# Kernel optimization log

Measured on AMD Instinct MI355X. Metric: run time of the kernel, lower is better.

The kernel has to match this reference:

```python
import jax, jax.numpy as jnp
import numpy as np

B, L, D_MODEL, H, D_K, D_V = 64, 52, 4096, 32, 128, 128
NEW_C = D_MODEL // H  # per-head input channel after the (faithful) raw reshape


def setup_inputs() -> dict:
    key = jax.random.key(0)
    ks = jax.random.split(key, 12)
    s = 0.02
    return {
        "Q": jax.random.normal(ks[0], (B, L, D_MODEL), jnp.float32),
        "K": jax.random.normal(ks[1], (B, L, D_MODEL), jnp.float32),
        "V": jax.random.normal(ks[2], (B, L, D_MODEL), jnp.float32),
        "Wq": jax.random.normal(ks[3], (H, NEW_C, D_K), jnp.float32) * s,
        "bq": jnp.zeros((H, D_K), jnp.float32),
        "Wk": jax.random.normal(ks[4], (H, NEW_C, D_K), jnp.float32) * s,
        "bk": jnp.zeros((H, D_K), jnp.float32),
        "Wv": jax.random.normal(ks[5], (H, NEW_C, D_V), jnp.float32) * s,
        "bv": jnp.zeros((H, D_V), jnp.float32),
        "Wo": jax.random.normal(ks[6], (H * D_V, D_MODEL), jnp.float32) * s,
        "bo": jnp.zeros((D_MODEL,), jnp.float32),
    }


def reference(Q, K, V, Wq, bq, Wk, bk, Wv, bv, Wo, bo):
    # Faithful to source: raw reshape (B, L, D) -> (B, H, L, D/H), NOT a channel split.
    def split(x):
        return x.reshape(B, H, L, NEW_C)

    q = jnp.einsum('bhlc,hck->bhlk', split(Q), Wq) + bq[None, :, None, :]  # (B,H,L,D_K)
    k = jnp.einsum('bhlc,hck->bhlk', split(K), Wk) + bk[None, :, None, :]
    v = jnp.einsum('bhlc,hcv->bhlv', split(V), Wv) + bv[None, :, None, :]

    scores = jnp.einsum('bhqk,bhmk->bhqm', q, k) / jnp.sqrt(jnp.asarray(D_K, q.dtype))
    # causal mask: keep j <= i, else -inf (matches the numpy masking loop)
    causal = jnp.tril(jnp.ones((L, L), bool))
    scores = jnp.where(causal[None, None], scores, -jnp.inf)
    attn = jax.nn.softmax(scores, axis=-1)
    o = jnp.einsum('bhqm,bhmv->bhqv', attn, v)  # (B,H,L,D_V)
    o = o.transpose(0, 2, 1, 3).reshape(B, L, H * D_V)  # concat heads on last axis
    # Dropout(0.1) is identity at inference.
    return o @ Wo + bo
```

## Files before the change

kernel.cpp:

```cpp
#include <hip/hip_runtime.h>
#include <hip/hip_bf16.h>

#define B_SZ   64
#define L_SZ   52
#define DMODEL 4096
#define H_SZ   32
#define C_SZ   128
#define DK     128

#define GM 3328
#define GN 4096
#define GK 4096

typedef __bf16 bf16x8 __attribute__((ext_vector_type(8)));
typedef float  f32x4  __attribute__((ext_vector_type(4)));

__device__ __forceinline__ void gload_lds16(const void* g, void* l) {
  __builtin_amdgcn_global_load_lds(
      (__attribute__((address_space(1))) void*)(void*)g,
      (__attribute__((address_space(3))) void*)l, 16, 0, 0);
}

__device__ __forceinline__ unsigned short bfbits(float x) {
  union { __hip_bfloat16 h; unsigned short u; } c;
  c.h = __float2bfloat16(x);
  return c.u;
}

__global__ __launch_bounds__(256) void w3_transpose_kernel(
    const float* __restrict__ Wq, const float* __restrict__ Wk,
    const float* __restrict__ Wv, __hip_bfloat16* __restrict__ WqT,
    __hip_bfloat16* __restrict__ WkT, __hip_bfloat16* __restrict__ WvT) {
  __shared__ float tile[64][65];
  const int bz = blockIdx.z;
  const float* in = (bz < 32 ? Wq : (bz < 64 ? Wk : Wv)) + (size_t)(bz & 31) * 16384;
  __hip_bfloat16* out = (bz < 32 ? WqT : (bz < 64 ? WkT : WvT)) + (size_t)(bz & 31) * 16384;
  const int nt = blockIdx.x, mt = blockIdx.y;
  const int t = threadIdx.x;
  const int r  = t >> 4;
  const int c4 = (t & 15) << 2;
#pragma unroll
  for (int p = 0; p < 4; ++p) {
    const int rr = r + p * 16;
    const float4 v = *(const float4*)(in + (size_t)(mt * 64 + rr) * 128 + nt * 64 + c4);
    tile[rr][c4 + 0] = v.x; tile[rr][c4 + 1] = v.y;
    tile[rr][c4 + 2] = v.z; tile[rr][c4 + 3] = v.w;
  }
  __syncthreads();
#pragma unroll
  for (int p = 0; p < 4; ++p) {
    const int rr = r + p * 16;
    union { __hip_bfloat16 h[4]; ushort4 u; } o4;
#pragma unroll
    for (int e = 0; e < 4; ++e) o4.h[e] = __float2bfloat16(tile[c4 + e][rr]);
    *(ushort4*)(out + (size_t)(nt * 64 + rr) * 128 + mt * 64 + c4) = o4.u;
  }
}

__device__ __forceinline__ void proj_lds(
    const __hip_bfloat16* __restrict__ xs, const __hip_bfloat16* __restrict__ WT,
    const float* __restrict__ bias, __hip_bfloat16* __restrict__ out,
    int n0, int r16, int kq) {
  f32x4 acc[4][2] = {};
  bf16x8 bfrag[2][4];
#pragma unroll
  for (int nt = 0; nt < 2; ++nt)
#pragma unroll
    for (int kk = 0; kk < 4; ++kk)
      bfrag[nt][kk] = *(const bf16x8*)(WT + (n0 + nt * 16 + r16) * 128 + kk * 32 + kq * 8);
#pragma unroll
  for (int kk = 0; kk < 4; ++kk) {
    bf16x8 a[4];
#pragma unroll
    for (int mt = 0; mt < 4; ++mt) {
      const int row = mt * 16 + r16;
      const int rowc = row < 52 ? row : 51;
      a[mt] = *(const bf16x8*)(xs + rowc * 136 + kk * 32 + kq * 8);
    }
#pragma unroll
    for (int mt = 0; mt < 4; ++mt)
#pragma unroll
      for (int nt = 0; nt < 2; ++nt)
        acc[mt][nt] = __builtin_amdgcn_mfma_f32_16x16x32_bf16(a[mt], bfrag[nt][kk], acc[mt][nt], 0, 0, 0);
  }
#pragma unroll
  for (int nt = 0; nt < 2; ++nt) {
    const int col = n0 + nt * 16 + r16;
    const float bv = bias[col];
#pragma unroll
    for (int mt = 0; mt < 4; ++mt) {
      const int m0 = mt * 16 + kq * 4;
      if (m0 < 52) {
#pragma unroll
        for (int i = 0; i < 4; ++i)
          if (m0 + i < 52)
            out[(m0 + i) * 136 + col] = __float2bfloat16(acc[mt][nt][i] + bv);
      }
    }
  }
}

__device__ __forceinline__ uint2 shfl64(uint2 v, int lane) {
  uint2 r;
  r.x = (unsigned)__shfl((int)v.x, lane);
  r.y = (unsigned)__shfl((int)v.y, lane);
  return r;
}

__global__ __launch_bounds__(256, 3) void attn_fused_kernel(
    const float* __restrict__ Qin, const float* __restrict__ Kin,
    const float* __restrict__ Vin,
    const __hip_bfloat16* __restrict__ WqT, const float* __restrict__ bq,
    const __hip_bfloat16* __restrict__ WkT, const float* __restrict__ bk,
    const __hip_bfloat16* __restrict__ WvT, const float* __restrict__ bv,
    __hip_bfloat16* __restrict__ Oc,
    const float* __restrict__ Wo, __hip_bfloat16* __restrict__ WoT) {
  __shared__ __align__(16) char lds[42432];
  const int gid = blockIdx.x;
  const int t = threadIdx.x;

  if (gid >= 2048) {
    float* tile = (float*)lds;
    const int bid2 = gid - 2048;
    const int nt = bid2 & 63, mt = bid2 >> 6;
    const int r  = t >> 4;
    const int c4 = (t & 15) << 2;
#pragma unroll
    for (int p = 0; p < 4; ++p) {
      const int rr = r + p * 16;
      const float4 v = *(const float4*)(Wo + (size_t)(mt * 64 + rr) * 4096 + nt * 64 + c4);
      tile[rr * 65 + c4 + 0] = v.x; tile[rr * 65 + c4 + 1] = v.y;
      tile[rr * 65 + c4 + 2] = v.z; tile[rr * 65 + c4 + 3] = v.w;
    }
    __syncthreads();
#pragma unroll
    for (int p = 0; p < 4; ++p) {
      const int rr = r + p * 16;
      union { __hip_bfloat16 h[4]; ushort4 u; } o4;
#pragma unroll
      for (int e = 0; e < 4; ++e) o4.h[e] = __float2bfloat16(tile[(c4 + e) * 65 + rr]);
      *(ushort4*)(WoT + (size_t)(nt * 64 + rr) * 4096 + mt * 64 + c4) = o4.u;
    }
    return;
  }

  __hip_bfloat16* r0 = (__hip_bfloat16*)(lds);
  __hip_bfloat16* r1 = (__hip_bfloat16*)(lds + 14144);
  __hip_bfloat16* r2 = (__hip_bfloat16*)(lds + 28288);
  float*          s_sh = (float*)(lds + 14144);
  __hip_bfloat16* p_sh = r0;

  const int h = gid & 31, bb = gid >> 5;
  const int lane = t & 63;
  const int w = t >> 6;
  const int r16 = lane & 15, kq = lane >> 4;
  const size_t xoff = (size_t)bb * (L_SZ * DMODEL) + (size_t)h * (L_SZ * C_SZ);
  const int n0 = w * 32;

  {
    const float* xp[3] = {Qin + xoff, Kin + xoff, Vin + xoff};
    __hip_bfloat16* xd[3] = {r0, r1, r2};
#pragma unroll
    for (int tz = 0; tz < 3; ++tz) {
      const float* X = xp[tz];
      __hip_bfloat16* xs = xd[tz];
      for (int idx = t; idx < 52 * 32; idx += 256) {
        const int row = idx >> 5, c4 = (idx & 31) << 2;
        const float4 v = *(const float4*)(X + row * 128 + c4);
        union { __hip_bfloat16 h[4]; ushort4 u; } o4;
        o4.h[0] = __float2bfloat16(v.x); o4.h[1] = __float2bfloat16(v.y);
        o4.h[2] = __float2bfloat16(v.z); o4.h[3] = __float2bfloat16(v.w);
        *(ushort4*)(xs + row * 136 + c4) = o4.u;
      }
    }
  }
  __syncthreads();

  uint2 vb[4][2];
  {
    f32x4 acc[4][2] = {};
    bf16x8 bfrag[2][4];
    const __hip_bfloat16* WT = WvT + (size_t)h * 16384;
#pragma unroll
    for (int nt = 0; nt < 2; ++nt)
#pragma unroll
      for (int kk = 0; kk < 4; ++kk)
        bfrag[nt][kk] = *(const bf16x8*)(WT + (n0 + nt * 16 + r16) * 128 + kk * 32 + kq * 8);
#pragma unroll
    for (int kk = 0; kk < 4; ++kk) {
      bf16x8 a[4];
#pragma unroll
      for (int mt = 0; mt < 4; ++mt) {
        const int row = mt * 16 + r16;
        const int rowc = row < 52 ? row : 51;
        a[mt] = *(const bf16x8*)(r2 + rowc * 136 + kk * 32 + kq * 8);
      }
#pragma unroll
      for (int mt = 0; mt < 4; ++mt)
#pragma unroll
        for (int nt = 0; nt < 2; ++nt)
          acc[mt][nt] = __builtin_amdgcn_mfma_f32_16x16x32_bf16(a[mt], bfrag[nt][kk], acc[mt][nt], 0, 0, 0);
    }
#pragma unroll
    for (int nt = 0; nt < 2; ++nt) {
      const float bvv = bv[h * 128 + n0 + nt * 16 + r16];
#pragma unroll
      for (int mt = 0; mt < 4; ++mt) {
        vb[mt][nt].x = (unsigned)bfbits(acc[mt][nt][0] + bvv) |
                       ((unsigned)bfbits(acc[mt][nt][1] + bvv) << 16);
        vb[mt][nt].y = (unsigned)bfbits(acc[mt][nt][2] + bvv) |
                       ((unsigned)bfbits(acc[mt][nt][3] + bvv) << 16);
      }
    }
  }
  __syncthreads();

  proj_lds(r0, WqT + (size_t)h * 16384, bq + h * 128, r2, n0, r16, kq);
  __syncthreads();

  proj_lds(r1, WkT + (size_t)h * 16384, bk + h * 128, r0, n0, r16, kq);
  __syncthreads();

  {
    const int nq = w * 16;
    f32x4 sacc[4] = {};
#pragma unroll
    for (int kk = 0; kk < 4; ++kk) {
      const int krow = nq + r16;
      const int krc = krow < 52 ? krow : 51;
      const bf16x8 bf_ = *(const bf16x8*)(r0 + krc * 136 + kk * 32 + kq * 8);
#pragma unroll
      for (int mt = 0; mt < 4; ++mt) {
        const int qrow = mt * 16 + r16;
        const int qrc = qrow < 52 ? qrow : 51;
        const bf16x8 a = *(const bf16x8*)(r2 + qrc * 136 + kk * 32 + kq * 8);
        sacc[mt] = __builtin_amdgcn_mfma_f32_16x16x32_bf16(a, bf_, sacc[mt], 0, 0, 0);
      }
    }
    const float scale = 0.08838834764831845f;
#pragma unroll
    for (int mt = 0; mt < 4; ++mt)
#pragma unroll
      for (int i = 0; i < 4; ++i) {
        const int row = mt * 16 + kq * 4 + i;
        if (row < 52) s_sh[row * 68 + nq + r16] = sacc[mt][i] * scale;
      }
  }
  __syncthreads();

  {
    const int r = t >> 2, qd = t & 3;
    if (r < 52) {
      float v[16];
      float mx = -3e38f;
#pragma unroll
      for (int j4 = 0; j4 < 4; ++j4) {
        const f32x4 s4 = *(const f32x4*)(s_sh + r * 68 + qd * 16 + j4 * 4);
#pragma unroll
        for (int e = 0; e < 4; ++e) {
          const int col = qd * 16 + j4 * 4 + e;
          const float val = (col <= r) ? s4[e] : -3e38f;
          v[j4 * 4 + e] = val;
          mx = fmaxf(mx, val);
        }
      }
      mx = fmaxf(mx, __shfl_xor(mx, 1));
      mx = fmaxf(mx, __shfl_xor(mx, 2));
      float ex[16];
      float sum = 0.f;
#pragma unroll
      for (int j = 0; j < 16; ++j) {
        const int col = qd * 16 + j;
        const float e = (col <= r) ? __expf(v[j] - mx) : 0.f;
        ex[j] = e; sum += e;
      }
      sum += __shfl_xor(sum, 1);
      sum += __shfl_xor(sum, 2);
      const float inv = 1.0f / sum;
      union { __hip_bfloat16 h[8]; uint4 q; } p0, p1;
#pragma unroll
      for (int j = 0; j < 8; ++j) {
        p0.h[j] = __float2bfloat16(ex[j] * inv);
        p1.h[j] = __float2bfloat16(ex[8 + j] * inv);
      }
      *(uint4*)(p_sh + r * 72 + qd * 16)     = p0.q;
      *(uint4*)(p_sh + r * 72 + qd * 16 + 8) = p1.q;
    }
  }
  __syncthreads();

  {
    const int half = (kq >> 1) & 1;
    const int src0 = ((kq & 1) << 5) + r16;
    const int src1 = src0 + 16;
    f32x4 oacc[4][2] = {};
#pragma unroll
    for (int kk = 0; kk < 2; ++kk) {
      bf16x8 bfr[2];
#pragma unroll
      for (int nt = 0; nt < 2; ++nt) {
        const uint2 a0 = shfl64(vb[2 * kk + 0][nt], src0);
        const uint2 a1 = shfl64(vb[2 * kk + 1][nt], src0);
        const uint2 b0 = shfl64(vb[2 * kk + 0][nt], src1);
        const uint2 b1 = shfl64(vb[2 * kk + 1][nt], src1);
        union { unsigned u[4]; bf16x8 v; } asm_;
        asm_.u[0] = half ? a1.x : a0.x;
        asm_.u[1] = half ? a1.y : a0.y;
        asm_.u[2] = half ? b1.x : b0.x;
        asm_.u[3] = half ? b1.y : b0.y;
        bfr[nt] = asm_.v;
      }
#pragma unroll
      for (int mt = 0; mt < 4; ++mt) {
        const int prow = mt * 16 + r16;
        const int prc = prow < 52 ? prow : 51;
        const bf16x8 a = *(const bf16x8*)(p_sh + prc * 72 + kk * 32 + kq * 8);
#pragma unroll
        for (int nt = 0; nt < 2; ++nt)
          oacc[mt][nt] = __builtin_amdgcn_mfma_f32_16x16x32_bf16(a, bfr[nt], oacc[mt][nt], 0, 0, 0);
      }
    }
    const size_t obase = (size_t)bb * 52 * 4096 + (size_t)h * 128;
#pragma unroll
    for (int nt = 0; nt < 2; ++nt) {
      const int col = n0 + nt * 16 + r16;
#pragma unroll
      for (int mt = 0; mt < 4; ++mt) {
        const int row0 = mt * 16 + kq * 4;
#pragma unroll
        for (int i = 0; i < 4; ++i) {
          const int row = row0 + i;
          if (row < 52)
            Oc[obase + (size_t)row * 4096 + col] = __float2bfloat16(oacc[mt][nt][i]);
        }
      }
    }
  }
}

#define STAGE(GBASE, REGOFF, KT, KS, WB) do {                                  \
    const __hip_bfloat16* s_ = (GBASE) + (size_t)(KT) * 64 + (KS) * 32;        \
    char* d_ = (WB) + (REGOFF) + ((KS) ? 16384 : 0) + t * 16;                  \
    gload_lds16(s_, d_);                                                       \
    gload_lds16(s_ + (size_t)128 * GK, d_ + 8192);                             \
  } while (0)

#define MFMA16(MQ, BF)                                                         \
  __builtin_amdgcn_sched_barrier(0);                                           \
  __builtin_amdgcn_s_setprio(1);                                               \
  _Pragma("unroll")                                                            \
  for (int mf = 0; mf < 4; ++mf)                                               \
    _Pragma("unroll")                                                          \
    for (int nf = 0; nf < 4; ++nf)                                             \
      acc[(MQ) * 4 + mf][nf] = __builtin_amdgcn_mfma_f32_16x16x32_bf16(        \
          af[mf], BF[nf], acc[(MQ) * 4 + mf][nf], 0, 0, 0);                    \
  __builtin_amdgcn_s_setprio(0)

#define READ_AF(RB, KS, MQ)                                                    \
  _Pragma("unroll")                                                            \
  for (int mf = 0; mf < 4; ++mf)                                               \
    af[mf] = *(const bf16x8*)((RB) + (KS) * 16384 + (MQ) * 4096 + aB0 + mf * 1024)

#define READ_BF(RB, BF, KS)                                                    \
  _Pragma("unroll")                                                            \
  for (int nf = 0; nf < 4; ++nf)                                               \
    BF[nf] = *(const bf16x8*)((RB) + 32768 + (KS) * 16384 + bB0 + nf * 1024)

#define KTILE_BODY(KT, RB, OB) do {                                            \
    const int s1 = (KT) + 1 < 64 ? (KT) + 1 : 63;                              \
    const int s2 = (KT) + 2 < 64 ? (KT) + 2 : 63;                              \
    {                                                                          \
      bf16x8 af[4];                                                            \
      READ_AF(RB, 0, 0);                                                       \
      READ_BF(RB, bf0, 0);                                                     \
      STAGE(gA0, 0, s1, 1, OB);                                                \
      __builtin_amdgcn_s_barrier();                                            \
      asm volatile("s_waitcnt lgkmcnt(0)" ::: "memory");                       \
      MFMA16(0, bf0);                                                          \
      __builtin_amdgcn_s_barrier();                                            \
    }                                                                          \
    {                                                                          \
      bf16x8 af[4];                                                            \
      READ_AF(RB, 0, 1);                                                       \
      STAGE(gB0, 32768, s2, 0, RB);                                            \
      __builtin_amdgcn_s_barrier();                                            \
      asm volatile("s_waitcnt lgkmcnt(0)" ::: "memory");                       \
      MFMA16(1, bf0);                                                          \
      __builtin_amdgcn_s_barrier();                                            \
    }                                                                          \
    {                                                                          \
      bf16x8 af[4];                                                            \
      READ_AF(RB, 1, 0);                                                       \
      READ_BF(RB, bf1, 1);                                                     \
      STAGE(gA0, 0, s2, 0, RB);                                                \
      __builtin_amdgcn_s_barrier();                                            \
      asm volatile("s_waitcnt lgkmcnt(0)" ::: "memory");                       \
      MFMA16(0, bf1);                                                          \
      __builtin_amdgcn_s_barrier();                                            \
    }                                                                          \
    {                                                                          \
      bf16x8 af[4];                                                            \
      READ_AF(RB, 1, 1);                                                       \
      STAGE(gB0, 32768, s2, 1, RB);                                            \
      __builtin_amdgcn_s_barrier();                                            \
      asm volatile("s_waitcnt lgkmcnt(0)" ::: "memory");                       \
      MFMA16(1, bf1);                                                          \
      asm volatile("s_waitcnt vmcnt(6)" ::: "memory");                         \
      __builtin_amdgcn_s_barrier();                                            \
    }                                                                          \
  } while (0)

__global__ __launch_bounds__(512, 2) void out_gemm_kernel(
    const __hip_bfloat16* __restrict__ A, const __hip_bfloat16* __restrict__ Bt,
    const float* __restrict__ bias, float* __restrict__ C) {
  __shared__ __align__(16) char lds[131072];

  int bid = blockIdx.x;
  bid = (bid & 7) * 26 + (bid >> 3);
  const int tm = bid >> 4;
  const int tn = bid & 15;

  const int t = threadIdx.x;
  const int w = t >> 6, lane = t & 63;
  const int wm = w >> 2, wn = w & 3;
  const int r16 = lane & 15, kq = lane >> 4;

  const int srow = t >> 2;
  const int sgslot = (t & 3) ^ ((srow >> 1) & 3);
  const __hip_bfloat16* gA0 = A  + (size_t)(tm * 256 + srow) * GK + sgslot * 8;
  const __hip_bfloat16* gB0 = Bt + (size_t)(tn * 256 + srow) * GK + sgslot * 8;

  const int slotr = kq ^ ((r16 >> 1) & 3);
  const int aB0 = (wm * 128 + r16) * 64 + slotr * 16;
  const int bB0 = (wn * 64 + r16) * 64 + slotr * 16;

  f32x4 acc[8][4] = {};
  bf16x8 bf0[4], bf1[4];

  char* const buf0 = lds;
  char* const buf1 = lds + 65536;

  STAGE(gA0, 0,     0, 0, buf0);
  STAGE(gA0, 0,     0, 1, buf0);
  STAGE(gB0, 32768, 0, 0, buf0);
  STAGE(gB0, 32768, 0, 1, buf0);
  STAGE(gB0, 32768, 1, 0, buf1);
  STAGE(gA0, 0,     1, 0, buf1);
  STAGE(gB0, 32768, 1, 1, buf1);
  asm volatile("s_waitcnt vmcnt(6)" ::: "memory");
  __builtin_amdgcn_s_barrier();

#pragma unroll 1
  for (int kt2 = 0; kt2 < 32; ++kt2) {
    const int kt = kt2 * 2;
    KTILE_BODY(kt,     buf0, buf1);
    KTILE_BODY(kt + 1, buf1, buf0);
  }
  asm volatile("s_waitcnt vmcnt(0) lgkmcnt(0)" ::: "memory");

  const int row0 = tm * 256 + wm * 128 + kq * 4;
  const int col0 = tn * 256 + wn * 64 + r16;
#pragma unroll
  for (int nf = 0; nf < 4; ++nf) {
    const int col = col0 + nf * 16;
    const float bv = bias[col];
#pragma unroll
    for (int mf = 0; mf < 8; ++mf) {
      const int row = row0 + mf * 16;
#pragma unroll
      for (int i = 0; i < 4; ++i)
        C[(size_t)(row + i) * GN + col] = acc[mf][nf][i] + bv;
    }
  }
}

extern "C" void kernel_launch(void* const* d_in, const int* in_sizes, int n_in,
                              void* d_out, int out_size, void* d_ws, size_t ws_size,
                              hipStream_t stream) {
  const float* Q  = (const float*)d_in[0];
  const float* K  = (const float*)d_in[1];
  const float* V  = (const float*)d_in[2];
  const float* Wq = (const float*)d_in[3];
  const float* bq = (const float*)d_in[4];
  const float* Wk = (const float*)d_in[5];
  const float* bk = (const float*)d_in[6];
  const float* Wv = (const float*)d_in[7];
  const float* bv = (const float*)d_in[8];
  const float* Wo = (const float*)d_in[9];
  const float* bo = (const float*)d_in[10];
  float* out = (float*)d_out;

  char* wsb = (char*)d_ws;
  __hip_bfloat16* WoT = (__hip_bfloat16*)wsb;
  __hip_bfloat16* Oc  = (__hip_bfloat16*)(wsb + (size_t)GN * GK * 2);
  __hip_bfloat16* WqT = (__hip_bfloat16*)(wsb + (size_t)GN * GK * 2 + (size_t)GM * GN * 2);
  __hip_bfloat16* WkT = WqT + (size_t)H_SZ * C_SZ * DK;
  __hip_bfloat16* WvT = WkT + (size_t)H_SZ * C_SZ * DK;

  w3_transpose_kernel<<<dim3(2, 2, 96), 256, 0, stream>>>(Wq, Wk, Wv, WqT, WkT, WvT);
  attn_fused_kernel<<<dim3(2048 + 4096), 256, 0, stream>>>(
      Q, K, V, WqT, bq, WkT, bk, WvT, bv, Oc, Wo, WoT);
  out_gemm_kernel<<<dim3(13 * 16), 512, 0, stream>>>(Oc, WoT, bo, out);
}
```

Baseline: 192.4 us.

## Swizzle attention LDS tiles and transpose MFMA operands for vectorized stores

Replaces padded LDS row strides with XOR-swizzled layouts for the Q/K/V, score and probability tiles. Those tiles shrink, so LDS per block drops and launch bounds rise from 3 to 4 blocks per CU. The Q/K projection and the P·V product swap MFMA operand order so each lane holds 4 consecutive columns. That allows packed 8-byte stores to LDS and to global Oc instead of scalar 2-byte stores. The aim is fewer bank conflicts, fewer store instructions and higher occupancy, at the risk of register pressure under the tighter launch bound.

```diff
diff --git a/kernel.cpp b/kernel.cpp
--- a/kernel.cpp
+++ b/kernel.cpp
@@ -25,6 +25,13 @@
   union { __hip_bfloat16 h; unsigned short u; } c;
   c.h = __float2bfloat16(x);
   return c.u;
+}
+
+__device__ __forceinline__ int hwoff(int row, int g) {
+  return row * 128 + ((g ^ (row & 7)) << 3);
+}
+__device__ __forceinline__ int wdoff(int row, int g) {
+  return row * 64 + ((g ^ (row & 7)) << 2);
 }
 
 __global__ __launch_bounds__(256) void w3_transpose_kernel(
@@ -57,44 +64,47 @@
   }
 }
 
-__device__ __forceinline__ void proj_lds(
+__device__ __forceinline__ void proj_swz(
     const __hip_bfloat16* __restrict__ xs, const __hip_bfloat16* __restrict__ WT,
     const float* __restrict__ bias, __hip_bfloat16* __restrict__ out,
     int n0, int r16, int kq) {
-  f32x4 acc[4][2] = {};
-  bf16x8 bfrag[2][4];
-#pragma unroll
-  for (int nt = 0; nt < 2; ++nt)
+  f32x4 acc[2][4] = {};
+  bf16x8 wf[2][4];
+#pragma unroll
+  for (int ct = 0; ct < 2; ++ct)
 #pragma unroll
     for (int kk = 0; kk < 4; ++kk)
-      bfrag[nt][kk] = *(const bf16x8*)(WT + (n0 + nt * 16 + r16) * 128 + kk * 32 + kq * 8);
+      wf[ct][kk] = *(const bf16x8*)(WT + (n0 + ct * 16 + r16) * 128 + kk * 32 + kq * 8);
 #pragma unroll
   for (int kk = 0; kk < 4; ++kk) {
-    bf16x8 a[4];
-#pragma unroll
-    for (int mt = 0; mt < 4; ++mt) {
-      const int row = mt * 16 + r16;
+    bf16x8 xf[4];
+#pragma unroll
+    for (int rt = 0; rt < 4; ++rt) {
+      const int row = rt * 16 + r16;
       const int rowc = row < 52 ? row : 51;
-      a[mt] = *(const bf16x8*)(xs + rowc * 136 + kk * 32 + kq * 8);
-    }
-#pragma unroll
-    for (int mt = 0; mt < 4; ++mt)
-#pragma unroll
-      for (int nt = 0; nt < 2; ++nt)
-        acc[mt][nt] = __builtin_amdgcn_mfma_f32_16x16x32_bf16(a[mt], bfrag[nt][kk], acc[mt][nt], 0, 0, 0);
-  }
-#pragma unroll
-  for (int nt = 0; nt < 2; ++nt) {
-    const int col = n0 + nt * 16 + r16;
-    const float bv = bias[col];
-#pragma unroll
-    for (int mt = 0; mt < 4; ++mt) {
-      const int m0 = mt * 16 + kq * 4;
-      if (m0 < 52) {
-#pragma unroll
-        for (int i = 0; i < 4; ++i)
-          if (m0 + i < 52)
-            out[(m0 + i) * 136 + col] = __float2bfloat16(acc[mt][nt][i] + bv);
+      xf[rt] = *(const bf16x8*)(xs + hwoff(rowc, 4 * kk + kq));
+    }
+#pragma unroll
+    for (int ct = 0; ct < 2; ++ct)
+#pragma unroll
+      for (int rt = 0; rt < 4; ++rt)
+        acc[ct][rt] = __builtin_amdgcn_mfma_f32_16x16x32_bf16(wf[ct][kk], xf[rt], acc[ct][rt], 0, 0, 0);
+  }
+#pragma unroll
+  for (int ct = 0; ct < 2; ++ct) {
+    const int col0 = n0 + ct * 16 + kq * 4;
+    const float4 b4 = *(const float4*)(bias + col0);
+    const int g = (n0 >> 3) + ct * 2 + (kq >> 1);
+#pragma unroll
+    for (int rt = 0; rt < 4; ++rt) {
+      const int row = rt * 16 + r16;
+      if (row < 52) {
+        ushort4 o;
+        o.x = bfbits(acc[ct][rt][0] + b4.x);
+        o.y = bfbits(acc[ct][rt][1] + b4.y);
+        o.z = bfbits(acc[ct][rt][2] + b4.z);
+        o.w = bfbits(acc[ct][rt][3] + b4.w);
+        *(ushort4*)(out + hwoff(row, g) + (kq & 1) * 4) = o;
       }
     }
   }
@@ -107,7 +117,7 @@
   return r;
 }
 
-__global__ __launch_bounds__(256, 3) void attn_fused_kernel(
+__global__ __launch_bounds__(256, 4) void attn_fused_kernel(
     const float* __restrict__ Qin, const float* __restrict__ Kin,
     const float* __restrict__ Vin,
     const __hip_bfloat16* __restrict__ WqT, const float* __restrict__ bq,
@@ -115,7 +125,7 @@
     const __hip_bfloat16* __restrict__ WvT, const float* __restrict__ bv,
     __hip_bfloat16* __restrict__ Oc,
     const float* __restrict__ Wo, __hip_bfloat16* __restrict__ WoT) {
-  __shared__ __align__(16) char lds[42432];
+  __shared__ __align__(16) char lds[39936];
   const int gid = blockIdx.x;
   const int t = threadIdx.x;
 
@@ -145,9 +155,9 @@
   }
 
   __hip_bfloat16* r0 = (__hip_bfloat16*)(lds);
-  __hip_bfloat16* r1 = (__hip_bfloat16*)(lds + 14144);
-  __hip_bfloat16* r2 = (__hip_bfloat16*)(lds + 28288);
-  float*          s_sh = (float*)(lds + 14144);
+  __hip_bfloat16* r1 = (__hip_bfloat16*)(lds + 13312);
+  __hip_bfloat16* r2 = (__hip_bfloat16*)(lds + 26624);
+  float*          s_sh = (float*)(lds + 13312);
   __hip_bfloat16* p_sh = r0;
 
   const int h = gid & 31, bb = gid >> 5;
@@ -170,7 +180,7 @@
         union { __hip_bfloat16 h[4]; ushort4 u; } o4;
         o4.h[0] = __float2bfloat16(v.x); o4.h[1] = __float2bfloat16(v.y);
         o4.h[2] = __float2bfloat16(v.z); o4.h[3] = __float2bfloat16(v.w);
-        *(ushort4*)(xs + row * 136 + c4) = o4.u;
+        *(ushort4*)(xs + hwoff(row, c4 >> 3) + (c4 & 4)) = o4.u;
       }
     }
   }
@@ -179,13 +189,13 @@
   uint2 vb[4][2];
   {
     f32x4 acc[4][2] = {};
-    bf16x8 bfrag[2][4];
+    bf16x8 wf[2][4];
     const __hip_bfloat16* WT = WvT + (size_t)h * 16384;
 #pragma unroll
-    for (int nt = 0; nt < 2; ++nt)
+    for (int ct = 0; ct < 2; ++ct)
 #pragma unroll
       for (int kk = 0; kk < 4; ++kk)
-        bfrag[nt][kk] = *(const bf16x8*)(WT + (n0 + nt * 16 + r16) * 128 + kk * 32 + kq * 8);
+        wf[ct][kk] = *(const bf16x8*)(WT + (n0 + ct * 16 + r16) * 128 + kk * 32 + kq * 8);
 #pragma unroll
     for (int kk = 0; kk < 4; ++kk) {
       bf16x8 a[4];
@@ -193,32 +203,32 @@
       for (int mt = 0; mt < 4; ++mt) {
         const int row = mt * 16 + r16;
         const int rowc = row < 52 ? row : 51;
-        a[mt] = *(const bf16x8*)(r2 + rowc * 136 + kk * 32 + kq * 8);
+        a[mt] = *(const bf16x8*)(r2 + hwoff(rowc, 4 * kk + kq));
       }
 #pragma unroll
       for (int mt = 0; mt < 4; ++mt)
 #pragma unroll
-        for (int nt = 0; nt < 2; ++nt)
-          acc[mt][nt] = __builtin_amdgcn_mfma_f32_16x16x32_bf16(a[mt], bfrag[nt][kk], acc[mt][nt], 0, 0, 0);
-    }
-#pragma unroll
-    for (int nt = 0; nt < 2; ++nt) {
-      const float bvv = bv[h * 128 + n0 + nt * 16 + r16];
+        for (int ct = 0; ct < 2; ++ct)
+          acc[mt][ct] = __builtin_amdgcn_mfma_f32_16x16x32_bf16(a[mt], wf[ct][kk], acc[mt][ct], 0, 0, 0);
+    }
+#pragma unroll
+    for (int ct = 0; ct < 2; ++ct) {
+      const float bvv = bv[h * 128 + n0 + ct * 16 + r16];
 #pragma unroll
       for (int mt = 0; mt < 4; ++mt) {
-        vb[mt][nt].x = (unsigned)bfbits(acc[mt][nt][0] + bvv) |
-                       ((unsigned)bfbits(acc[mt][nt][1] + bvv) << 16);
-        vb[mt][nt].y = (unsigned)bfbits(acc[mt][nt][2] + bvv) |
-                       ((unsigned)bfbits(acc[mt][nt][3] + bvv) << 16);
-      }
-    }
-  }
-  __syncthreads();
-
-  proj_lds(r0, WqT + (size_t)h * 16384, bq + h * 128, r2, n0, r16, kq);
-  __syncthreads();
-
-  proj_lds(r1, WkT + (size_t)h * 16384, bk + h * 128, r0, n0, r16, kq);
+        vb[mt][ct].x = (unsigned)bfbits(acc[mt][ct][0] + bvv) |
+                       ((unsigned)bfbits(acc[mt][ct][1] + bvv) << 16);
+        vb[mt][ct].y = (unsigned)bfbits(acc[mt][ct][2] + bvv) |
+                       ((unsigned)bfbits(acc[mt][ct][3] + bvv) << 16);
+      }
+    }
+  }
+  __syncthreads();
+
+  proj_swz(r0, WqT + (size_t)h * 16384, bq + h * 128, r2, n0, r16, kq);
+  __syncthreads();
+
+  proj_swz(r1, WkT + (size_t)h * 16384, bk + h * 128, r0, n0, r16, kq);
   __syncthreads();
 
   {
@@ -228,22 +238,23 @@
     for (int kk = 0; kk < 4; ++kk) {
       const int krow = nq + r16;
       const int krc = krow < 52 ? krow : 51;
-      const bf16x8 bf_ = *(const bf16x8*)(r0 + krc * 136 + kk * 32 + kq * 8);
+      const bf16x8 kf = *(const bf16x8*)(r0 + hwoff(krc, 4 * kk + kq));
 #pragma unroll
       for (int mt = 0; mt < 4; ++mt) {
         const int qrow = mt * 16 + r16;
         const int qrc = qrow < 52 ? qrow : 51;
-        const bf16x8 a = *(const bf16x8*)(r2 + qrc * 136 + kk * 32 + kq * 8);
-        sacc[mt] = __builtin_amdgcn_mfma_f32_16x16x32_bf16(a, bf_, sacc[mt], 0, 0, 0);
+        const bf16x8 a = *(const bf16x8*)(r2 + hwoff(qrc, 4 * kk + kq));
+        sacc[mt] = __builtin_amdgcn_mfma_f32_16x16x32_bf16(a, kf, sacc[mt], 0, 0, 0);
       }
     }
     const float scale = 0.08838834764831845f;
+    const int c = nq + r16;
 #pragma unroll
     for (int mt = 0; mt < 4; ++mt)
 #pragma unroll
       for (int i = 0; i < 4; ++i) {
         const int row = mt * 16 + kq * 4 + i;
-        if (row < 52) s_sh[row * 68 + nq + r16] = sacc[mt][i] * scale;
+        if (row < 52) s_sh[wdoff(row, c >> 2) + (c & 3)] = sacc[mt][i] * scale;
       }
   }
   __syncthreads();
@@ -255,7 +266,7 @@
       float mx = -3e38f;
 #pragma unroll
       for (int j4 = 0; j4 < 4; ++j4) {
-        const f32x4 s4 = *(const f32x4*)(s_sh + r * 68 + qd * 16 + j4 * 4);
+        const f32x4 s4 = *(const f32x4*)(s_sh + wdoff(r, qd * 4 + j4));
 #pragma unroll
         for (int e = 0; e < 4; ++e) {
           const int col = qd * 16 + j4 * 4 + e;
@@ -283,8 +294,8 @@
         p0.h[j] = __float2bfloat16(ex[j] * inv);
         p1.h[j] = __float2bfloat16(ex[8 + j] * inv);
       }
-      *(uint4*)(p_sh + r * 72 + qd * 16)     = p0.q;
-      *(uint4*)(p_sh + r * 72 + qd * 16 + 8) = p1.q;
+      *(uint4*)(p_sh + hwoff(r, qd * 2))     = p0.q;
+      *(uint4*)(p_sh + hwoff(r, qd * 2 + 1)) = p1.q;
     }
   }
   __syncthreads();
@@ -293,45 +304,50 @@
     const int half = (kq >> 1) & 1;
     const int src0 = ((kq & 1) << 5) + r16;
     const int src1 = src0 + 16;
-    f32x4 oacc[4][2] = {};
+    f32x4 oaccT[2][4] = {};
 #pragma unroll
     for (int kk = 0; kk < 2; ++kk) {
       bf16x8 bfr[2];
 #pragma unroll
-      for (int nt = 0; nt < 2; ++nt) {
-        const uint2 a0 = shfl64(vb[2 * kk + 0][nt], src0);
-        const uint2 a1 = shfl64(vb[2 * kk + 1][nt], src0);
-        const uint2 b0 = shfl64(vb[2 * kk + 0][nt], src1);
-        const uint2 b1 = shfl64(vb[2 * kk + 1][nt], src1);
+      for (int ct = 0; ct < 2; ++ct) {
+        const uint2 a0 = shfl64(vb[2 * kk + 0][ct], src0);
+        const uint2 a1 = shfl64(vb[2 * kk + 1][ct], src0);
+        const uint2 b0 = shfl64(vb[2 * kk + 0][ct], src1);
+        const uint2 b1 = shfl64(vb[2 * kk + 1][ct], src1);
         union { unsigned u[4]; bf16x8 v; } asm_;
         asm_.u[0] = half ? a1.x : a0.x;
         asm_.u[1] = half ? a1.y : a0.y;
         asm_.u[2] = half ? b1.x : b0.x;
         asm_.u[3] = half ? b1.y : b0.y;
-        bfr[nt] = asm_.v;
-      }
-#pragma unroll
-      for (int mt = 0; mt < 4; ++mt) {
-        const int prow = mt * 16 + r16;
+        bfr[ct] = asm_.v;
+      }
+      bf16x8 pf[4];
+#pragma unroll
+      for (int rt = 0; rt < 4; ++rt) {
+        const int prow = rt * 16 + r16;
         const int prc = prow < 52 ? prow : 51;
-        const bf16x8 a = *(const bf16x8*)(p_sh + prc * 72 + kk * 32 + kq * 8);
-#pragma unroll
-        for (int nt = 0; nt < 2; ++nt)
-          oacc[mt][nt] = __builtin_amdgcn_mfma_f32_16x16x32_bf16(a, bfr[nt], oacc[mt][nt], 0, 0, 0);
-      }
+        pf[rt] = *(const bf16x8*)(p_sh + hwoff(prc, 4 * kk + kq));
+      }
+#pragma unroll
+      for (int ct = 0; ct < 2; ++ct)
+#pragma unroll
+        for (int rt = 0; rt < 4; ++rt)
+          oaccT[ct][rt] = __builtin_amdgcn_mfma_f32_16x16x32_bf16(bfr[ct], pf[rt], oaccT[ct][rt], 0, 0, 0);
     }
     const size_t obase = (size_t)bb * 52 * 4096 + (size_t)h * 128;
 #pragma unroll
-    for (int nt = 0; nt < 2; ++nt) {
-      const int col = n0 + nt * 16 + r16;
-#pragma unroll
-      for (int mt = 0; mt < 4; ++mt) {
-        const int row0 = mt * 16 + kq * 4;
-#pragma unroll
-        for (int i = 0; i < 4; ++i) {
-          const int row = row0 + i;
-          if (row < 52)
-            Oc[obase + (size_t)row * 4096 + col] = __float2bfloat16(oacc[mt][nt][i]);
+    for (int ct = 0; ct < 2; ++ct) {
+      const int col0 = n0 + ct * 16 + kq * 4;
+#pragma unroll
+      for (int rt = 0; rt < 4; ++rt) {
+        const int row = rt * 16 + r16;
+        if (row < 52) {
+          ushort4 o;
+          o.x = bfbits(oaccT[ct][rt][0]);
+          o.y = bfbits(oaccT[ct][rt][1]);
+          o.z = bfbits(oaccT[ct][rt][2]);
+          o.w = bfbits(oaccT[ct][rt][3]);
+          *(ushort4*)(Oc + obase + (size_t)row * 4096 + col0) = o;
         }
       }
     }
```

Result: slower. 196.5 us (+2.1%).
